# Kernel optimization log

Hardware: AMD Instinct MI355X
Metric: run time of the kernel (lower is better)

The kernel has to match this reference:

```python
import jax, jax.numpy as jnp
import numpy as np

N_NODES = 100000
HIDDEN = 8
N_EDGES = 16000000


def setup_inputs() -> dict:
    key = jax.random.key(0)
    k1, k2, k3, k4, k5 = jax.random.split(key, 5)
    z_demand = jax.random.normal(k1, (N_NODES, HIDDEN), dtype=jnp.float32)
    z_measurement = jax.random.normal(k2, (N_NODES, HIDDEN), dtype=jnp.float32)
    edge_label_index = jax.random.randint(k3, (2, N_EDGES), 0, N_NODES, dtype=jnp.int64)
    # Linear(16 -> 8) and Linear(8 -> 1), stored as [in, out] for x @ W + b
    w1 = jax.random.normal(k4, (2 * HIDDEN, HIDDEN), dtype=jnp.float32) * (1.0 / np.sqrt(2 * HIDDEN))
    b1 = jnp.zeros((HIDDEN,), dtype=jnp.float32)
    w2 = jax.random.normal(k5, (HIDDEN, 1), dtype=jnp.float32) * (1.0 / np.sqrt(HIDDEN))
    b2 = jnp.zeros((1,), dtype=jnp.float32)
    return {
        "z_demand": z_demand,
        "z_measurement": z_measurement,
        "edge_label_index": edge_label_index,
        "w1": w1,
        "b1": b1,
        "w2": w2,
        "b2": b2,
    }


def reference(z_demand, z_measurement, edge_label_index, w1, b1, w2, b2) -> jnp.ndarray:
    row = edge_label_index[0]  # [E] indices into demand table
    col = edge_label_index[1]  # [E] indices into measurement table
    # gather + concat: [E, 2*HIDDEN]
    z = jnp.concatenate([z_demand[row], z_measurement[col]], axis=-1)
    h = jax.nn.relu(z @ w1 + b1)          # [E, HIDDEN]
    logits = h @ w2 + b2                  # [E, 1]
    out = jax.nn.sigmoid(logits)          # sigmoid=True path
    return out.reshape(-1)                # [E]
```

## Files before the change

### kernel.cpp

```cpp
#include <hip/hip_runtime.h>
#include <math.h>

#define HIDDEN 8

__global__ __launch_bounds__(256) void convert_kernel(
    const float* __restrict__ zd, const float* __restrict__ zm,
    unsigned* __restrict__ zdb, unsigned* __restrict__ zmb, int npairs)
{
    int i = blockIdx.x * blockDim.x + threadIdx.x;
    const float* src;
    unsigned* dst;
    int p;
    if (i < npairs) {
        src = zd; dst = zdb; p = i;
    } else if (i < 2 * npairs) {
        src = zm; dst = zmb; p = i - npairs;
    } else {
        return;
    }
    union { float f; unsigned u; } lo, hi;
    lo.f = src[2 * p];
    hi.f = src[2 * p + 1];
    unsigned lr = (lo.u + 0x7fffu + ((lo.u >> 16) & 1u)) >> 16;
    unsigned hr = (hi.u + 0x7fffu + ((hi.u >> 16) & 1u)) & 0xffff0000u;
    dst[p] = lr | hr;
}

__global__ __launch_bounds__(256) void edge_decoder_bf16_kernel(
    const unsigned* __restrict__ zdb,
    const unsigned* __restrict__ zmb,
    const int* __restrict__ row, const int* __restrict__ col,
    const float* __restrict__ w1, const float* __restrict__ b1,
    const float* __restrict__ w2, const float* __restrict__ b2,
    float* __restrict__ out, int E, int N)
{
    int i = blockIdx.x * blockDim.x + threadIdx.x;
    if (i >= E) return;

    int r = row[i];
    int c = col[i];
    if (r < 0) r = 0;
    if (r > N - 1) r = N - 1;
    if (c < 0) c = 0;
    if (c > N - 1) c = N - 1;

    const unsigned* ar = zdb + (size_t)r * 4;
    const unsigned* mc = zmb + (size_t)c * 4;

    unsigned pk[8];
#pragma unroll
    for (int k = 0; k < 4; ++k) pk[k] = ar[k];
#pragma unroll
    for (int k = 0; k < 4; ++k) pk[4 + k] = mc[k];

    float z[16];
#pragma unroll
    for (int k = 0; k < 8; ++k) {
        union { unsigned u; float f; } a, b;
        a.u = pk[k] << 16;
        b.u = pk[k] & 0xffff0000u;
        z[2 * k] = a.f;
        z[2 * k + 1] = b.f;
    }

    float h[HIDDEN];
#pragma unroll
    for (int j = 0; j < HIDDEN; ++j) h[j] = b1[j];
#pragma unroll
    for (int k = 0; k < 2 * HIDDEN; ++k) {
        float zk = z[k];
#pragma unroll
        for (int j = 0; j < HIDDEN; ++j)
            h[j] = fmaf(zk, w1[k * HIDDEN + j], h[j]);
    }

    float logit = b2[0];
#pragma unroll
    for (int j = 0; j < HIDDEN; ++j) {
        float hj = h[j] > 0.0f ? h[j] : 0.0f;
        logit = fmaf(hj, w2[j], logit);
    }

    out[i] = 1.0f / (1.0f + expf(-logit));
}

__global__ __launch_bounds__(256) void edge_decoder_f32_kernel(
    const float* __restrict__ zd, const float* __restrict__ zm,
    const int* __restrict__ row, const int* __restrict__ col,
    const float* __restrict__ w1, const float* __restrict__ b1,
    const float* __restrict__ w2, const float* __restrict__ b2,
    float* __restrict__ out, int E, int N)
{
    int i = blockIdx.x * blockDim.x + threadIdx.x;
    if (i >= E) return;
    int r = row[i];
    int c = col[i];
    if (r < 0) r = 0;
    if (r > N - 1) r = N - 1;
    if (c < 0) c = 0;
    if (c > N - 1) c = N - 1;
    const float* zdr = zd + (size_t)r * HIDDEN;
    const float* zmc = zm + (size_t)c * HIDDEN;
    float z[16];
#pragma unroll
    for (int k = 0; k < HIDDEN; ++k) z[k] = zdr[k];
#pragma unroll
    for (int k = 0; k < HIDDEN; ++k) z[HIDDEN + k] = zmc[k];
    float h[HIDDEN];
#pragma unroll
    for (int j = 0; j < HIDDEN; ++j) h[j] = b1[j];
#pragma unroll
    for (int k = 0; k < 2 * HIDDEN; ++k) {
        float zk = z[k];
#pragma unroll
        for (int j = 0; j < HIDDEN; ++j)
            h[j] = fmaf(zk, w1[k * HIDDEN + j], h[j]);
    }
    float logit = b2[0];
#pragma unroll
    for (int j = 0; j < HIDDEN; ++j) {
        float hj = h[j] > 0.0f ? h[j] : 0.0f;
        logit = fmaf(hj, w2[j], logit);
    }
    out[i] = 1.0f / (1.0f + expf(-logit));
}

extern "C" void kernel_launch(void* const* d_in, const int* in_sizes, int n_in,
                              void* d_out, int out_size, void* d_ws, size_t ws_size,
                              hipStream_t stream) {
    const float* zd  = (const float*)d_in[0];
    const float* zm  = (const float*)d_in[1];
    const int*   eli = (const int*)d_in[2];
    const float* w1  = (const float*)d_in[3];
    const float* b1  = (const float*)d_in[4];
    const float* w2  = (const float*)d_in[5];
    const float* b2  = (const float*)d_in[6];
    float* out = (float*)d_out;

    int E = out_size;
    int N = in_sizes[0] / HIDDEN;
    if (E <= 0 || N <= 0) return;

    const int* row = eli;
    const int* col = eli + E;
    const int block = 256;

    size_t tbl_bytes = (size_t)N * 4 * sizeof(unsigned);
    if (ws_size >= 2 * tbl_bytes) {
        unsigned* zdb = (unsigned*)d_ws;
        unsigned* zmb = zdb + (size_t)N * 4;

        int npairs = N * 4;
        int cgrid = (2 * npairs + block - 1) / block;
        convert_kernel<<<cgrid, block, 0, stream>>>(zd, zm, zdb, zmb, npairs);

        int grid = (E + block - 1) / block;
        edge_decoder_bf16_kernel<<<grid, block, 0, stream>>>(
            zdb, zmb, row, col, w1, b1, w2, b2, out, E, N);
    } else {
        int grid = (E + block - 1) / block;
        edge_decoder_f32_kernel<<<grid, block, 0, stream>>>(
            zd, zm, row, col, w1, b1, w2, b2, out, E, N);
    }
}
```

Before: 349.5 us.

## Precompute per-node first-layer projections so edges only add and apply ReLU

The first linear layer is linear in the concatenated inputs, so each node's contribution (z_demand·W1_top and z_measurement·W1_bottom + b1) is now computed once per node and stored as bf16 tables. Each edge then gathers the two projected vectors, adds them, applies ReLU and the second layer. This removes the 128 FMAs per edge and keeps the gather size unchanged. The cost is that rounding to bf16 now happens on the projected values rather than the raw inputs, which changes numerical error slightly.

```diff
diff --git a/kernel.cpp b/kernel.cpp
--- a/kernel.cpp
+++ b/kernel.cpp
@@ -3,34 +3,60 @@
 
 #define HIDDEN 8
 
-__global__ __launch_bounds__(256) void convert_kernel(
+__device__ __forceinline__ unsigned pack_bf16_pair(float lo, float hi) {
+    union { float f; unsigned u; } a, b;
+    a.f = lo; b.f = hi;
+    unsigned lr = (a.u + 0x7fffu + ((a.u >> 16) & 1u)) >> 16;
+    unsigned hr = (b.u + 0x7fffu + ((b.u >> 16) & 1u)) & 0xffff0000u;
+    return lr | hr;
+}
+
+__global__ __launch_bounds__(256) void precompute_uv_kernel(
     const float* __restrict__ zd, const float* __restrict__ zm,
-    unsigned* __restrict__ zdb, unsigned* __restrict__ zmb, int npairs)
+    const float* __restrict__ w1, const float* __restrict__ b1,
+    unsigned* __restrict__ u, unsigned* __restrict__ v, int N)
 {
     int i = blockIdx.x * blockDim.x + threadIdx.x;
-    const float* src;
-    unsigned* dst;
-    int p;
-    if (i < npairs) {
-        src = zd; dst = zdb; p = i;
-    } else if (i < 2 * npairs) {
-        src = zm; dst = zmb; p = i - npairs;
-    } else {
-        return;
+    if (i < N) {
+        float x[HIDDEN];
+#pragma unroll
+        for (int k = 0; k < HIDDEN; ++k) x[k] = zd[i * HIDDEN + k];
+        float acc[HIDDEN];
+#pragma unroll
+        for (int j = 0; j < HIDDEN; ++j) acc[j] = 0.0f;
+#pragma unroll
+        for (int k = 0; k < HIDDEN; ++k) {
+#pragma unroll
+            for (int j = 0; j < HIDDEN; ++j)
+                acc[j] = fmaf(x[k], w1[k * HIDDEN + j], acc[j]);
+        }
+#pragma unroll
+        for (int p = 0; p < 4; ++p)
+            u[i * 4 + p] = pack_bf16_pair(acc[2 * p], acc[2 * p + 1]);
+    } else if (i < 2 * N) {
+        int q = i - N;
+        float x[HIDDEN];
+#pragma unroll
+        for (int k = 0; k < HIDDEN; ++k) x[k] = zm[q * HIDDEN + k];
+        float acc[HIDDEN];
+#pragma unroll
+        for (int j = 0; j < HIDDEN; ++j) acc[j] = b1[j];
+#pragma unroll
+        for (int k = 0; k < HIDDEN; ++k) {
+#pragma unroll
+            for (int j = 0; j < HIDDEN; ++j)
+                acc[j] = fmaf(x[k], w1[(HIDDEN + k) * HIDDEN + j], acc[j]);
+        }
+#pragma unroll
+        for (int p = 0; p < 4; ++p)
+            v[q * 4 + p] = pack_bf16_pair(acc[2 * p], acc[2 * p + 1]);
     }
-    union { float f; unsigned u; } lo, hi;
-    lo.f = src[2 * p];
-    hi.f = src[2 * p + 1];
-    unsigned lr = (lo.u + 0x7fffu + ((lo.u >> 16) & 1u)) >> 16;
-    unsigned hr = (hi.u + 0x7fffu + ((hi.u >> 16) & 1u)) & 0xffff0000u;
-    dst[p] = lr | hr;
 }
 
-__global__ __launch_bounds__(256) void edge_decoder_bf16_kernel(
-    const unsigned* __restrict__ zdb,
-    const unsigned* __restrict__ zmb,
+__global__ __launch_bounds__(256) void edge_decoder_uv_kernel(
+    const unsigned* __restrict__ u,
+    const unsigned* __restrict__ v,
     const int* __restrict__ row, const int* __restrict__ col,
-    const float* __restrict__ w1, const float* __restrict__ b1,
     const float* __restrict__ w2, const float* __restrict__ b2,
     float* __restrict__ out, int E, int N)
 {
@@ -44,41 +70,29 @@
     if (c < 0) c = 0;
     if (c > N - 1) c = N - 1;
 
-    const unsigned* ar = zdb + (size_t)r * 4;
-    const unsigned* mc = zmb + (size_t)c * 4;
+    const unsigned* ur = u + (size_t)r * 4;
+    const unsigned* vc = v + (size_t)c * 4;
 
-    unsigned pk[8];
+    unsigned pu[4], pv[4];
 #pragma unroll
-    for (int k = 0; k < 4; ++k) pk[k] = ar[k];
+    for (int k = 0; k < 4; ++k) pu[k] = ur[k];
 #pragma unroll
-    for (int k = 0; k < 4; ++k) pk[4 + k] = mc[k];
-
-    float z[16];
-#pragma unroll
-    for (int k = 0; k < 8; ++k) {
-        union { unsigned u; float f; } a, b;
-        a.u = pk[k] << 16;
-        b.u = pk[k] & 0xffff0000u;
-        z[2 * k] = a.f;
-        z[2 * k + 1] = b.f;
-    }
-
-    float h[HIDDEN];
-#pragma unroll
-    for (int j = 0; j < HIDDEN; ++j) h[j] = b1[j];
-#pragma unroll
-    for (int k = 0; k < 2 * HIDDEN; ++k) {
-        float zk = z[k];
-#pragma unroll
-        for (int j = 0; j < HIDDEN; ++j)
-            h[j] = fmaf(zk, w1[k * HIDDEN + j], h[j]);
-    }
+    for (int k = 0; k < 4; ++k) pv[k] = vc[k];
 
     float logit = b2[0];
 #pragma unroll
-    for (int j = 0; j < HIDDEN; ++j) {
-        float hj = h[j] > 0.0f ? h[j] : 0.0f;
-        logit = fmaf(hj, w2[j], logit);
+    for (int k = 0; k < 4; ++k) {
+        union { unsigned q; float f; } a0, a1, b0, b1u;
+        a0.q = pu[k] << 16;
+        a1.q = pu[k] & 0xffff0000u;
+        b0.q = pv[k] << 16;
+        b1u.q = pv[k] & 0xffff0000u;
+        float h0 = a0.f + b0.f;
+        float h1 = a1.f + b1u.f;
+        if (h0 < 0.0f) h0 = 0.0f;
+        if (h1 < 0.0f) h1 = 0.0f;
+        logit = fmaf(h0, w2[2 * k], logit);
+        logit = fmaf(h1, w2[2 * k + 1], logit);
     }
 
     out[i] = 1.0f / (1.0f + expf(-logit));
@@ -147,16 +161,15 @@
 
     size_t tbl_bytes = (size_t)N * 4 * sizeof(unsigned);
     if (ws_size >= 2 * tbl_bytes) {
-        unsigned* zdb = (unsigned*)d_ws;
-        unsigned* zmb = zdb + (size_t)N * 4;
+        unsigned* u = (unsigned*)d_ws;
+        unsigned* v = u + (size_t)N * 4;
 
-        int npairs = N * 4;
-        int cgrid = (2 * npairs + block - 1) / block;
-        convert_kernel<<<cgrid, block, 0, stream>>>(zd, zm, zdb, zmb, npairs);
+        int pgrid = (2 * N + block - 1) / block;
+        precompute_uv_kernel<<<pgrid, block, 0, stream>>>(zd, zm, w1, b1, u, v, N);
 
         int grid = (E + block - 1) / block;
-        edge_decoder_bf16_kernel<<<grid, block, 0, stream>>>(
-            zdb, zmb, row, col, w1, b1, w2, b2, out, E, N);
+        edge_decoder_uv_kernel<<<grid, block, 0, stream>>>(
+            u, v, row, col, w2, b2, out, E, N);
     } else {
         int grid = (E + block - 1) / block;
         edge_decoder_f32_kernel<<<grid, block, 0, stream>>>(
```

Measured after the change: 313.8 us. 10.2% less time.
